# Kernel tuning notes

Measured on AMD Instinct MI355X. Metric: run time of the kernel, lower is better.

## Reference

```python
import jax, jax.numpy as jnp
import numpy as np

BETA = 50.0
SIGMA = 5.0


def l2_normalize(x, axis=1):
    # matches torch: norm = (sum(x^2) + 1e-6) ** 0.5
    return x / jnp.sqrt(jnp.sum(x * x, axis=axis, keepdims=True) + 1e-6)


def matching_layer(f1, f2):
    # corr[b, j, i] = <f2[:, j], f1[:, i]>, shaped (b, h2*w2, h1, w1)
    f1 = l2_normalize(f1, 1)
    f2 = l2_normalize(f2, 1)
    b, c, h, w = f1.shape
    corr = jnp.einsum('bcj,bci->bji', f2.reshape(b, c, h * w), f1.reshape(b, c, h * w))
    return jax.nn.relu(corr).reshape(b, h * w, h, w)


def kernel_soft_argmax(corr, beta=BETA, sigma=SIGMA):
    b, hw, h, w = corr.shape
    # gaussian kernel centered at argmax over the target-position axis (dim 1)
    idx = jnp.argmax(corr, axis=1)                      # (b, h, w)
    idx_y = (idx // w).astype(corr.dtype)[:, None, None]  # (b,1,1,h,w)
    idx_x = (idx % w).astype(corr.dtype)[:, None, None]
    xs = jnp.arange(w, dtype=corr.dtype).reshape(1, 1, w, 1, 1)
    ys = jnp.arange(h, dtype=corr.dtype).reshape(1, h, 1, 1, 1)
    gauss = jnp.exp(-((xs - idx_x) ** 2 + (ys - idx_y) ** 2) / (2.0 * sigma ** 2))
    corr = gauss.reshape(b, hw, h, w) * corr
    # softmax with temperature over dim 1 (stable: subtract max, then exp(beta*x))
    m = jnp.max(corr, axis=1, keepdims=True)
    e = jnp.exp(beta * (corr - m))
    p = e / jnp.sum(e, axis=1, keepdims=True)
    p = p.reshape(b, h, w, h, w)
    x_normal = jnp.linspace(-1.0, 1.0, w, dtype=corr.dtype).reshape(1, w, 1, 1)
    y_normal = jnp.linspace(-1.0, 1.0, h, dtype=corr.dtype).reshape(1, h, 1, 1)
    grid_x = jnp.sum(jnp.sum(p, axis=1) * x_normal, axis=1, keepdims=True)  # (b,1,h,w)
    grid_y = jnp.sum(jnp.sum(p, axis=2) * y_normal, axis=1, keepdims=True)  # (b,1,h,w)
    return grid_x, grid_y


def find_correspondence(corr):
    grid_x, grid_y = kernel_soft_argmax(corr)
    grid = jnp.concatenate([jnp.transpose(grid_x, (0, 2, 3, 1)),
                            jnp.transpose(grid_y, (0, 2, 3, 1))], axis=3)  # (b,h,w,2)
    # faithful to source: flow = grid_x - grid_x == zeros
    flow = jnp.concatenate([grid_x - grid_x, grid_y - grid_y], axis=1)  # (b,2,h,w)
    return grid, flow


def setup_inputs() -> dict:
    key = jax.random.key(0)
    k1, k2, k3, k4 = jax.random.split(key, 4)
    return {
        'src_feat3': jax.random.normal(k1, (2, 1024, 64, 64), dtype=jnp.float32),
        'tgt_feat3': jax.random.normal(k2, (2, 1024, 64, 64), dtype=jnp.float32),
        'src_feat4': jax.random.normal(k3, (2, 2048, 64, 64), dtype=jnp.float32),
        'tgt_feat4': jax.random.normal(k4, (2, 2048, 64, 64), dtype=jnp.float32),
    }


def reference(src_feat3, tgt_feat3, src_feat4, tgt_feat4):
    corr3 = matching_layer(src_feat3, tgt_feat3)  # (b, hw, h, w)
    corr4 = matching_layer(src_feat4, tgt_feat4)
    b, hw, h, w = corr3.shape
    corr_s2t = l2_normalize(corr3 * corr4, axis=1)
    # transpose source/target axes for t2s
    corr3_t = jnp.transpose(corr3.reshape(b, hw, hw), (0, 2, 1)).reshape(b, hw, h, w)
    corr4_t = jnp.transpose(corr4.reshape(b, hw, hw), (0, 2, 1)).reshape(b, hw, h, w)
    corr_t2s = l2_normalize(corr3_t * corr4_t, axis=1)
    grid_s2t, flow_s2t = find_correspondence(corr_s2t)
    grid_t2s, flow_t2s = find_correspondence(corr_t2s)
    return grid_s2t, flow_s2t, grid_t2s, flow_t2s
```

## Files before the change

### kernel.cpp

```cpp
#include <hip/hip_runtime.h>
#include <math.h>

#define HW 4096
#define FIXUP_THR 4e-3f

typedef _Float16 half8_t __attribute__((ext_vector_type(8)));
typedef _Float16 half4_t __attribute__((ext_vector_type(4)));
typedef float f32x4 __attribute__((ext_vector_type(4)));

__global__ __launch_bounds__(256) void transpose_half(const float* __restrict__ f,
                                                      _Float16* __restrict__ out,
                                                      float* __restrict__ part,
                                                      int C, int b) {
    __shared__ float tile[64][65];
    const int t = threadIdx.x;
    const int p0 = blockIdx.x * 64;
    const int c0 = blockIdx.y * 64;
    const float* src = f + ((size_t)b * C + c0) * HW + p0;
    {
        const int cl = t >> 4;
        const int pl = (t & 15) * 4;
#pragma unroll
        for (int it = 0; it < 4; ++it) {
            float4 v = *(const float4*)(src + (size_t)(cl + it * 16) * HW + pl);
            tile[cl + it * 16][pl + 0] = v.x;
            tile[cl + it * 16][pl + 1] = v.y;
            tile[cl + it * 16][pl + 2] = v.z;
            tile[cl + it * 16][pl + 3] = v.w;
        }
    }
    __syncthreads();
    const int pr = t >> 3;
    const int cb = (t & 7) * 8;
#pragma unroll
    for (int it = 0; it < 2; ++it) {
        const int p = pr + it * 32;
        union { _Float16 h[8]; float4 v4; } H;
        float ssq = 0.f;
#pragma unroll
        for (int u = 0; u < 8; ++u) {
            float v = tile[cb + u][p];
            H.h[u] = (_Float16)v;
            ssq = fmaf(v, v, ssq);
        }
        *(float4*)(out + (size_t)(p0 + p) * C + c0 + cb) = H.v4;
        ssq += __shfl_down(ssq, 4);
        ssq += __shfl_down(ssq, 2);
        ssq += __shfl_down(ssq, 1);
        if ((t & 7) == 0) part[(size_t)blockIdx.y * 4096 + p0 + p] = ssq;
    }
}

__global__ __launch_bounds__(256) void norm_finalize_b(const float* __restrict__ part,
                                                       float* __restrict__ inv, int b) {
    const int idx = blockIdx.x * 256 + threadIdx.x;
    const int tensor = idx >> 12;
    const int pos = idx & 4095;
    const int nblk[4] = {16, 16, 32, 32};
    const int poff[4] = {0, 65536, 131072, 262144};
    const int ivoff[4] = {8192, 0, 24576, 16384};
    const float* pt = part + poff[tensor] + pos;
    float s = 0.f;
    const int n = nblk[tensor];
    for (int k = 0; k < n; ++k) s += pt[(size_t)k * 4096];
    inv[ivoff[tensor] + b * 4096 + pos] = 1.0f / sqrtf(s + 1e-6f);
}

__global__ __launch_bounds__(256, 3) void corr_fused(
    const _Float16* __restrict__ A3, const _Float16* __restrict__ B3,
    const _Float16* __restrict__ A4, const _Float16* __restrict__ B4,
    const float* __restrict__ invA3, const float* __restrict__ invB3,
    const float* __restrict__ invA4, const float* __restrict__ invB4,
    _Float16* __restrict__ M, _Float16* __restrict__ MT, int b) {
    __shared__ char lds[32768];
    const int tid = threadIdx.x;
    const int i0 = blockIdx.x * 128;
    const int j0 = blockIdx.y * 128;
    const int lane = tid & 63;
    const int w = tid >> 6;
    const int wj = (w >> 1) * 64, wi = (w & 1) * 64;
    const int quad = lane >> 4;

    int offA[2][4], offB[2][4];
#pragma unroll
    for (int f = 0; f < 4; ++f) {
        int jr = wj + f * 16 + (lane & 15);
        int baseA = jr * 128 + ((quad ^ (jr & 3)) << 4);
        int xkA = ((jr >> 2) & 1) << 6;
        offA[0][f] = baseA + xkA;
        offA[1][f] = baseA + (64 ^ xkA);
        int ir = wi + f * 16 + (lane & 15);
        int baseB = 16384 + ir * 128 + ((quad ^ (ir & 3)) << 4);
        int xkB = ((ir >> 2) & 1) << 6;
        offB[0][f] = baseB + xkB;
        offB[1][f] = baseB + (64 ^ xkB);
    }

    int srow[8], selem[8];
#pragma unroll
    for (int s = 0; s < 8; ++s) {
        int g = s * 256 + tid;
        srow[s] = (g >> 3) & 127;
        selem[s] = ((g & 7) ^ (srow[s] & 7)) << 3;
    }

    half4_t v3p[4][4];
    f32x4 acc[4][4] = {};

#pragma unroll
    for (int ph = 0; ph < 2; ++ph) {
        const _Float16* Ap = ph ? A4 : A3;
        const _Float16* Bp = ph ? B4 : B3;
        const int C = ph ? 2048 : 1024;
        const _Float16* srcs[8];
#pragma unroll
        for (int s = 0; s < 8; ++s) {
            const _Float16* pl = (s < 4) ? Ap : Bp;
            int rbase = (s < 4) ? j0 : i0;
            srcs[s] = pl + (size_t)(rbase + srow[s]) * C + selem[s];
        }
#pragma unroll 1
        for (int kt = 0; kt < C; kt += 64) {
#pragma unroll
            for (int s = 0; s < 8; ++s) {
                __builtin_amdgcn_global_load_lds(
                    (const __attribute__((address_space(1))) void*)(srcs[s]),
                    (__attribute__((address_space(3))) void*)(lds + (s * 256 + tid) * 16),
                    16, 0, 0);
                srcs[s] += 64;
            }
            __syncthreads();
#pragma unroll
            for (int st = 0; st < 2; ++st) {
                half8_t a[4], bb[4];
#pragma unroll
                for (int f = 0; f < 4; ++f) {
                    a[f] = *(const half8_t*)(lds + offA[st][f]);
                    bb[f] = *(const half8_t*)(lds + offB[st][f]);
                }
#pragma unroll
                for (int fy = 0; fy < 4; ++fy)
#pragma unroll
                    for (int fx = 0; fx < 4; ++fx)
                        acc[fy][fx] = __builtin_amdgcn_mfma_f32_16x16x32_f16(
                            a[fy], bb[fx], acc[fy][fx], 0, 0, 0);
            }
            __syncthreads();
        }
        if (ph == 0) {
            const int ib = i0 + wi + (lane & 15);
            float sB[4];
#pragma unroll
            for (int fx = 0; fx < 4; ++fx) sB[fx] = invB3[b * 4096 + ib + fx * 16];
#pragma unroll
            for (int fy = 0; fy < 4; ++fy) {
                const int jb = j0 + wj + fy * 16 + quad * 4;
                float sA[4];
#pragma unroll
                for (int r = 0; r < 4; ++r) sA[r] = invA3[b * 4096 + jb + r];
#pragma unroll
                for (int fx = 0; fx < 4; ++fx)
#pragma unroll
                    for (int r = 0; r < 4; ++r) {
                        v3p[fy][fx][r] =
                            (_Float16)fmaxf(acc[fy][fx][r] * sA[r] * sB[fx], 0.f);
                        acc[fy][fx][r] = 0.f;
                    }
            }
        }
    }

    const int ib = i0 + wi + (lane & 15);
    float sB[4];
#pragma unroll
    for (int fx = 0; fx < 4; ++fx) sB[fx] = invB4[b * 4096 + ib + fx * 16];
#pragma unroll
    for (int fy = 0; fy < 4; ++fy) {
        const int jb = j0 + wj + fy * 16 + quad * 4;
        float sA[4];
#pragma unroll
        for (int r = 0; r < 4; ++r) sA[r] = invA4[b * 4096 + jb + r];
#pragma unroll
        for (int fx = 0; fx < 4; ++fx) {
            const int ii = ib + fx * 16;
            union { _Float16 h[4]; double d; } pk;
#pragma unroll
            for (int r = 0; r < 4; ++r) {
                float v = fmaxf(acc[fy][fx][r] * sA[r] * sB[fx], 0.f) *
                          (float)v3p[fy][fx][r];
                M[((size_t)b * HW + (jb + r)) * HW + ii] = (_Float16)v;
                pk.h[r] = (_Float16)v;
            }
            *(double*)(MT + ((size_t)b * HW + ii) * HW + jb) = pk.d;
        }
    }
}

__device__ __forceinline__ void top2_merge(float& a1, int& ai1, float& a2, int& ai2,
                                           float b1, int bi1, float b2, int bi2) {
    float n1, n2;
    int ni1, ni2;
    bool bfirst = (b1 > a1) || (b1 == a1 && bi1 < ai1);
    if (bfirst) {
        n1 = b1; ni1 = bi1;
        if (a1 > b2 || (a1 == b2 && ai1 < bi2)) { n2 = a1; ni2 = ai1; }
        else { n2 = b2; ni2 = bi2; }
    } else {
        n1 = a1; ni1 = ai1;
        if (b1 > a2 || (b1 == a2 && bi1 < ai2)) { n2 = b1; ni2 = bi1; }
        else { n2 = a2; ni2 = ai2; }
    }
    a1 = n1; ai1 = ni1; a2 = n2; ai2 = ni2;
}

__global__ __launch_bounds__(256, 6) void soft_argmax(
    const _Float16* __restrict__ M, const _Float16* __restrict__ MT,
    float* __restrict__ out,
    const float* __restrict__ s3, const float* __restrict__ t3,
    const float* __restrict__ s4, const float* __restrict__ t4,
    const float* __restrict__ inv) {
    __shared__ _Float16 bufh[HW];
    __shared__ float lf[3072];
    __shared__ float gtab[128];
    __shared__ float wsA[4], wsB[4], wsC[4];
    __shared__ int wiA[4], wiB[4];
    __shared__ int cnd[64];
    __shared__ int ncnd;
    __shared__ float bestE;
    __shared__ int bestI;
    const int tid = threadIdx.x;
    const int lane = tid & 63;
    const int wv = tid >> 6;
    const int b = blockIdx.y;
    const int line = blockIdx.x;
    const int colmode = blockIdx.z;

    const float* cf3 = colmode ? t3 : s3;
    const float* lf3 = colmode ? s3 : t3;
    const float* cf4 = colmode ? t4 : s4;
    const float* lf4 = colmode ? s4 : t4;
    const float* invc3 = inv + (colmode ? 8192 : 0);
    const float* invl3 = inv + (colmode ? 0 : 8192);
    const float* invc4 = inv + (colmode ? 24576 : 16384);
    const float* invl4 = inv + (colmode ? 16384 : 24576);

    const _Float16* src = (colmode ? MT : M) + ((size_t)b * HW + line) * HW;
    const half8_t* s8 = (const half8_t*)src;

    float ss = 0.f, v1 = -1.f, v2 = -1.f;
    int i1 = 0, i2 = 0;
#pragma unroll
    for (int it = 0; it < 2; ++it) {
        const int j8 = tid + it * 256;
        half8_t h = s8[j8];
        *(half8_t*)(bufh + j8 * 8) = h;
#pragma unroll
        for (int u = 0; u < 8; ++u) {
            float v = (float)h[u];
            int j = j8 * 8 + u;
            ss = fmaf(v, v, ss);
            if (v > v1) { v2 = v1; i2 = i1; v1 = v; i1 = j; }
            else if (v > v2) { v2 = v; i2 = j; }
        }
    }
#pragma unroll
    for (int m = 1; m < 64; m <<= 1) {
        ss += __shfl_xor(ss, m);
        float b1 = __shfl_xor(v1, m); int bi1 = __shfl_xor(i1, m);
        float b2 = __shfl_xor(v2, m); int bi2 = __shfl_xor(i2, m);
        top2_merge(v1, i1, v2, i2, b1, bi1, b2, bi2);
    }
    if (lane == 0) { wsA[wv] = ss; wsB[wv] = v1; wiA[wv] = i1; wsC[wv] = v2; wiB[wv] = i2; }
    __syncthreads();
    float ssq = wsA[0] + wsA[1] + wsA[2] + wsA[3];
    float m1 = wsB[0], m2 = wsC[0];
    int mi1 = wiA[0], mi2 = wiB[0];
#pragma unroll
    for (int k = 1; k < 4; ++k)
        top2_merge(m1, mi1, m2, mi2, wsB[k], wiA[k], wsC[k], wiB[k]);
    const float inv_l = 1.0f / sqrtf(ssq + 1e-6f);
    const float vmax = m1 * inv_l;
    int amax = mi1;
    (void)mi2;

    const float cut = m1 - FIXUP_THR * m1;
    if (m2 >= cut) {
        if (tid == 0) { ncnd = 0; bestE = -1.f; bestI = 1 << 30; }
        __syncthreads();
        for (int j = tid; j < HW; j += 256)
            if ((float)bufh[j] >= cut) {
                int k = atomicAdd(&ncnd, 1);
                if (k < 64) cnd[k] = j;
            }
        for (int c = tid; c < 1024; c += 256)
            lf[c] = lf3[((size_t)b * 1024 + c) * HW + line];
        for (int c = tid; c < 2048; c += 256)
            lf[1024 + c] = lf4[((size_t)b * 2048 + c) * HW + line];
        __syncthreads();
        int nc = ncnd < 64 ? ncnd : 64;
#pragma unroll 1
        for (int k = 0; k < nc; ++k) {
            int jc = cnd[k];
            float d3 = 0.f, d4 = 0.f;
            for (int c = tid; c < 1024; c += 256)
                d3 = fmaf(cf3[((size_t)b * 1024 + c) * HW + jc], lf[c], d3);
            for (int c = tid; c < 2048; c += 256)
                d4 = fmaf(cf4[((size_t)b * 2048 + c) * HW + jc], lf[1024 + c], d4);
#pragma unroll
            for (int m = 1; m < 64; m <<= 1) {
                d3 += __shfl_xor(d3, m);
                d4 += __shfl_xor(d4, m);
            }
            if (lane == 0) { wsA[wv] = d3; wsB[wv] = d4; }
            __syncthreads();
            if (tid == 0) {
                float s3d = wsA[0] + wsA[1] + wsA[2] + wsA[3];
                float s4d = wsB[0] + wsB[1] + wsB[2] + wsB[3];
                float e3 = fmaxf(s3d * invc3[b * 4096 + jc] * invl3[b * 4096 + line], 0.f);
                float e4 = fmaxf(s4d * invc4[b * 4096 + jc] * invl4[b * 4096 + line], 0.f);
                float e = e3 * e4;
                if (e > bestE || (e == bestE && jc < bestI)) { bestE = e; bestI = jc; }
            }
            __syncthreads();
        }
        amax = bestI;
    }

    const float ax = (float)(amax & 63);
    const float ay = (float)(amax >> 6);

    if (tid < 128) {
        float d = (float)(tid & 63) - ((tid < 64) ? ax : ay);
        gtab[tid] = __expf(-d * d * 0.02f);
    }
    __syncthreads();

    float se = 0.f, sx = 0.f, sy = 0.f;
#pragma unroll
    for (int it = 0; it < 2; ++it) {
        const int j8 = tid + it * 256;
        half8_t h = *(const half8_t*)(bufh + j8 * 8);
        const int x0 = (j8 & 7) * 8;
        const int y2 = j8 >> 3;
        const float gyi = gtab[64 + y2] * inv_l;
        const float yn = fmaf((float)y2, 2.0f / 63.0f, -1.0f);
        float sec = 0.f;
#pragma unroll
        for (int u = 0; u < 8; ++u) {
            float v = gtab[x0 + u] * (float)h[u] * gyi;
            float e = __expf(50.0f * (v - vmax));
            sec += e;
            sx = fmaf(e, fmaf((float)(x0 + u), 2.0f / 63.0f, -1.0f), sx);
        }
        se += sec;
        sy = fmaf(sec, yn, sy);
    }
#pragma unroll
    for (int m = 1; m < 64; m <<= 1) {
        se += __shfl_xor(se, m);
        sx += __shfl_xor(sx, m);
        sy += __shfl_xor(sy, m);
    }
    if (lane == 0) { wsA[wv] = se; wsB[wv] = sx; wsC[wv] = sy; }
    __syncthreads();
    if (tid == 0) {
        float S = wsA[0] + wsA[1] + wsA[2] + wsA[3];
        float X = wsB[0] + wsB[1] + wsB[2] + wsB[3];
        float Y = wsC[0] + wsC[1] + wsC[2] + wsC[3];
        float gx = X / S;
        float gy = Y / S;
        size_t gbase = colmode ? 0 : 32768;
        size_t fbase = colmode ? 16384 : 49152;
        size_t p = gbase + ((size_t)b * HW + line) * 2;
        out[p] = gx;
        out[p + 1] = gy;
        out[fbase + (size_t)(b * 2 + 0) * HW + line] = 0.f;
        out[fbase + (size_t)(b * 2 + 1) * HW + line] = 0.f;
    }
}

extern "C" void kernel_launch(void* const* d_in, const int* in_sizes, int n_in,
                              void* d_out, int out_size, void* d_ws, size_t ws_size,
                              hipStream_t stream) {
    const float* s3 = (const float*)d_in[0];
    const float* t3 = (const float*)d_in[1];
    const float* s4 = (const float*)d_in[2];
    const float* t4 = (const float*)d_in[3];
    float* out = (float*)d_out;
    char* base = (char*)d_ws;

    float* inv = (float*)base;
    float* part = (float*)(base + 131072);
    _Float16* M16 = (_Float16*)(base + 1703936);
    _Float16* MT16 = (_Float16*)(base + 68812800);
    _Float16* P = (_Float16*)(base + 135921664);
    _Float16* P3t = P;
    _Float16* P3s = P + 4194304;
    _Float16* P4t = P + 8388608;
    _Float16* P4s = P + 16777216;

    dim3 t3g(64, 16), t4g(64, 32), gg(32, 32);
    for (int b = 0; b < 2; ++b) {
        transpose_half<<<t3g, 256, 0, stream>>>(t3, P3t, part + 0, 1024, b);
        transpose_half<<<t3g, 256, 0, stream>>>(s3, P3s, part + 65536, 1024, b);
        transpose_half<<<t4g, 256, 0, stream>>>(t4, P4t, part + 131072, 2048, b);
        transpose_half<<<t4g, 256, 0, stream>>>(s4, P4s, part + 262144, 2048, b);
        norm_finalize_b<<<64, 256, 0, stream>>>(part, inv, b);
        corr_fused<<<gg, 256, 0, stream>>>(P3t, P3s, P4t, P4s,
                                           inv + 8192, inv + 0, inv + 24576, inv + 16384,
                                           M16, MT16, b);
    }

    dim3 rg(4096, 2, 2);
    soft_argmax<<<rg, 256, 0, stream>>>(M16, MT16, out, s3, t3, s4, t4, inv);
}
```

Measured before the change: 659.6 us.

## Double-buffer LDS in correlation GEMM and merge transpose launches into one

The correlation kernel now uses two 32KB LDS buffers and prefetches the next K-tile with global_load_lds while computing the current one. The prefetch crosses from the layer-3 to the layer-4 operands without a drain. This removes one barrier per tile and hides global load latency. It also doubles LDS per block and lowers the occupancy hint from 3 to 2 blocks per CU. Separately, the four per-tensor transpose launches per batch are folded into a single launch that dispatches on block index, cutting launch overhead and tail effects.

New measurement: 572.3 us. -13.2%, faster.

```diff
diff --git a/kernel.cpp b/kernel.cpp
--- a/kernel.cpp
+++ b/kernel.cpp
@@ -8,14 +8,29 @@
 typedef _Float16 half4_t __attribute__((ext_vector_type(4)));
 typedef float f32x4 __attribute__((ext_vector_type(4)));
 
-__global__ __launch_bounds__(256) void transpose_half(const float* __restrict__ f,
-                                                      _Float16* __restrict__ out,
-                                                      float* __restrict__ part,
-                                                      int C, int b) {
+__global__ __launch_bounds__(256) void transpose_b(
+    const float* __restrict__ s3f, const float* __restrict__ t3f,
+    const float* __restrict__ s4f, const float* __restrict__ t4f,
+    _Float16* __restrict__ P, float* __restrict__ part, int b) {
     __shared__ float tile[64][65];
     const int t = threadIdx.x;
-    const int p0 = blockIdx.x * 64;
-    const int c0 = blockIdx.y * 64;
+    int blk = blockIdx.x;
+    const float* f;
+    _Float16* out;
+    float* pt;
+    int C;
+    if (blk < 2048) {
+        C = 1024;
+        if (blk < 1024) { f = t3f; out = P;            pt = part;          }
+        else            { f = s3f; out = P + 4194304;  pt = part + 65536;  blk -= 1024; }
+    } else {
+        C = 2048;
+        if (blk < 4096) { f = t4f; out = P + 8388608;  pt = part + 131072; blk -= 2048; }
+        else            { f = s4f; out = P + 16777216; pt = part + 262144; blk -= 4096; }
+    }
+    const int p0 = (blk & 63) * 64;
+    const int c0 = (blk >> 6) * 64;
+    const int cblk = blk >> 6;
     const float* src = f + ((size_t)b * C + c0) * HW + p0;
     {
         const int cl = t >> 4;
@@ -47,7 +62,7 @@
         ssq += __shfl_down(ssq, 4);
         ssq += __shfl_down(ssq, 2);
         ssq += __shfl_down(ssq, 1);
-        if ((t & 7) == 0) part[(size_t)blockIdx.y * 4096 + p0 + p] = ssq;
+        if ((t & 7) == 0) pt[(size_t)cblk * 4096 + p0 + p] = ssq;
     }
 }
 
@@ -66,13 +81,13 @@
     inv[ivoff[tensor] + b * 4096 + pos] = 1.0f / sqrtf(s + 1e-6f);
 }
 
-__global__ __launch_bounds__(256, 3) void corr_fused(
+__global__ __launch_bounds__(256, 2) void corr_fused(
     const _Float16* __restrict__ A3, const _Float16* __restrict__ B3,
     const _Float16* __restrict__ A4, const _Float16* __restrict__ B4,
     const float* __restrict__ invA3, const float* __restrict__ invB3,
     const float* __restrict__ invA4, const float* __restrict__ invB4,
     _Float16* __restrict__ M, _Float16* __restrict__ MT, int b) {
-    __shared__ char lds[32768];
+    __shared__ char lds[65536];
     const int tid = threadIdx.x;
     const int i0 = blockIdx.x * 128;
     const int j0 = blockIdx.y * 128;
@@ -104,70 +119,92 @@
         selem[s] = ((g & 7) ^ (srow[s] & 7)) << 3;
     }
 
+    const _Float16* s3p[8];
+    const _Float16* s4p[8];
+#pragma unroll
+    for (int s = 0; s < 8; ++s) {
+        if (s < 4) {
+            s3p[s] = A3 + (size_t)(j0 + srow[s]) * 1024 + selem[s];
+            s4p[s] = A4 + (size_t)(j0 + srow[s]) * 2048 + selem[s];
+        } else {
+            s3p[s] = B3 + (size_t)(i0 + srow[s]) * 1024 + selem[s];
+            s4p[s] = B4 + (size_t)(i0 + srow[s]) * 2048 + selem[s];
+        }
+    }
+
     half4_t v3p[4][4];
     f32x4 acc[4][4] = {};
 
-#pragma unroll
-    for (int ph = 0; ph < 2; ++ph) {
-        const _Float16* Ap = ph ? A4 : A3;
-        const _Float16* Bp = ph ? B4 : B3;
-        const int C = ph ? 2048 : 1024;
-        const _Float16* srcs[8];
+    auto stage = [&](int buf, const _Float16** sp) {
 #pragma unroll
         for (int s = 0; s < 8; ++s) {
-            const _Float16* pl = (s < 4) ? Ap : Bp;
-            int rbase = (s < 4) ? j0 : i0;
-            srcs[s] = pl + (size_t)(rbase + srow[s]) * C + selem[s];
-        }
+            __builtin_amdgcn_global_load_lds(
+                (const __attribute__((address_space(1))) void*)(sp[s]),
+                (__attribute__((address_space(3))) void*)(lds + (buf << 15) +
+                                                          (s * 256 + tid) * 16),
+                16, 0, 0);
+            sp[s] += 64;
+        }
+    };
+    auto compute = [&](int buf) {
+        const int bo = buf << 15;
+#pragma unroll
+        for (int st = 0; st < 2; ++st) {
+            half8_t a[4], bb[4];
+#pragma unroll
+            for (int f = 0; f < 4; ++f) {
+                a[f] = *(const half8_t*)(lds + bo + offA[st][f]);
+                bb[f] = *(const half8_t*)(lds + bo + offB[st][f]);
+            }
+#pragma unroll
+            for (int fy = 0; fy < 4; ++fy)
+#pragma unroll
+                for (int fx = 0; fx < 4; ++fx)
+                    acc[fy][fx] = __builtin_amdgcn_mfma_f32_16x16x32_f16(
+                        a[fy], bb[fx], acc[fy][fx], 0, 0, 0);
+        }
+    };
+
+    stage(0, s3p);
+    __syncthreads();
+    int cur = 0;
 #pragma unroll 1
-        for (int kt = 0; kt < C; kt += 64) {
-#pragma unroll
-            for (int s = 0; s < 8; ++s) {
-                __builtin_amdgcn_global_load_lds(
-                    (const __attribute__((address_space(1))) void*)(srcs[s]),
-                    (__attribute__((address_space(3))) void*)(lds + (s * 256 + tid) * 16),
-                    16, 0, 0);
-                srcs[s] += 64;
-            }
-            __syncthreads();
-#pragma unroll
-            for (int st = 0; st < 2; ++st) {
-                half8_t a[4], bb[4];
-#pragma unroll
-                for (int f = 0; f < 4; ++f) {
-                    a[f] = *(const half8_t*)(lds + offA[st][f]);
-                    bb[f] = *(const half8_t*)(lds + offB[st][f]);
+    for (int kt = 0; kt < 16; ++kt) {
+        if (kt < 15) stage(cur ^ 1, s3p);
+        else         stage(cur ^ 1, s4p);
+        compute(cur);
+        __syncthreads();
+        cur ^= 1;
+    }
+
+    {
+        const int ib = i0 + wi + (lane & 15);
+        float sB[4];
+#pragma unroll
+        for (int fx = 0; fx < 4; ++fx) sB[fx] = invB3[b * 4096 + ib + fx * 16];
+#pragma unroll
+        for (int fy = 0; fy < 4; ++fy) {
+            const int jb = j0 + wj + fy * 16 + quad * 4;
+            float sA[4];
+#pragma unroll
+            for (int r = 0; r < 4; ++r) sA[r] = invA3[b * 4096 + jb + r];
+#pragma unroll
+            for (int fx = 0; fx < 4; ++fx)
+#pragma unroll
+                for (int r = 0; r < 4; ++r) {
+                    v3p[fy][fx][r] =
+                        (_Float16)fmaxf(acc[fy][fx][r] * sA[r] * sB[fx], 0.f);
+                    acc[fy][fx][r] = 0.f;
                 }
-#pragma unroll
-                for (int fy = 0; fy < 4; ++fy)
-#pragma unroll
-                    for (int fx = 0; fx < 4; ++fx)
-                        acc[fy][fx] = __builtin_amdgcn_mfma_f32_16x16x32_f16(
-                            a[fy], bb[fx], acc[fy][fx], 0, 0, 0);
-            }
-            __syncthreads();
-        }
-        if (ph == 0) {
-            const int ib = i0 + wi + (lane & 15);
-            float sB[4];
-#pragma unroll
-            for (int fx = 0; fx < 4; ++fx) sB[fx] = invB3[b * 4096 + ib + fx * 16];
-#pragma unroll
-            for (int fy = 0; fy < 4; ++fy) {
-                const int jb = j0 + wj + fy * 16 + quad * 4;
-                float sA[4];
-#pragma unroll
-                for (int r = 0; r < 4; ++r) sA[r] = invA3[b * 4096 + jb + r];
-#pragma unroll
-                for (int fx = 0; fx < 4; ++fx)
-#pragma unroll
-                    for (int r = 0; r < 4; ++r) {
-                        v3p[fy][fx][r] =
-                            (_Float16)fmaxf(acc[fy][fx][r] * sA[r] * sB[fx], 0.f);
-                        acc[fy][fx][r] = 0.f;
-                    }
-            }
-        }
+        }
+    }
+
+#pragma unroll 1
+    for (int kt = 0; kt < 32; ++kt) {
+        if (kt < 31) stage(cur ^ 1, s4p);
+        compute(cur);
+        __syncthreads();
+        cur ^= 1;
     }
 
     const int ib = i0 + wi + (lane & 15);
@@ -394,19 +431,12 @@
     _Float16* M16 = (_Float16*)(base + 1703936);
     _Float16* MT16 = (_Float16*)(base + 68812800);
     _Float16* P = (_Float16*)(base + 135921664);
-    _Float16* P3t = P;
-    _Float16* P3s = P + 4194304;
-    _Float16* P4t = P + 8388608;
-    _Float16* P4s = P + 16777216;
-
-    dim3 t3g(64, 16), t4g(64, 32), gg(32, 32);
+
+    dim3 gg(32, 32);
     for (int b = 0; b < 2; ++b) {
-        transpose_half<<<t3g, 256, 0, stream>>>(t3, P3t, part + 0, 1024, b);
-        transpose_half<<<t3g, 256, 0, stream>>>(s3, P3s, part + 65536, 1024, b);
-        transpose_half<<<t4g, 256, 0, stream>>>(t4, P4t, part + 131072, 2048, b);
-        transpose_half<<<t4g, 256, 0, stream>>>(s4, P4s, part + 262144, 2048, b);
+        transpose_b<<<6144, 256, 0, stream>>>(s3, t3, s4, t4, P, part, b);
         norm_finalize_b<<<64, 256, 0, stream>>>(part, inv, b);
-        corr_fused<<<gg, 256, 0, stream>>>(P3t, P3s, P4t, P4s,
+        corr_fused<<<gg, 256, 0, stream>>>(P, P + 4194304, P + 8388608, P + 16777216,
                                            inv + 8192, inv + 0, inv + 24576, inv + 16384,
                                            M16, MT16, b);
     }
```
